# Kernel tuning notes

Measured on AMD Instinct MI355X. Metric: run time of the kernel, lower is better.

## Reference

```python
import jax, jax.numpy as jnp
import numpy as np

B, S, H, T, N = 32, 512, 1024, 8, 16


def setup_inputs() -> dict:
    key = jax.random.key(0)
    ks = jax.random.split(key, 16)
    sc = 1.0 / np.sqrt(H)
    f32 = jnp.float32
    return {
        "hidden": jax.random.normal(ks[0], (S, B, H), f32),
        "num_encoder_outputs": jax.random.normal(ks[1], (B, N, H), f32),
        "problem_q": jax.random.normal(ks[2], (B, H), f32),
        # GenerateXQs K/V projections
        "Wk": jax.random.normal(ks[3], (H, H), f32) * sc,
        "bk": jax.random.normal(ks[4], (H,), f32) * sc,
        "Wv": jax.random.normal(ks[5], (H, H), f32) * sc,
        "bv": jax.random.normal(ks[6], (H,), f32) * sc,
        # XToQ K/V projections
        "Wk2": jax.random.normal(ks[7], (H, H), f32) * sc,
        "bk2": jax.random.normal(ks[8], (H,), f32) * sc,
        "Wv2": jax.random.normal(ks[9], (H, H), f32) * sc,
        "bv2": jax.random.normal(ks[10], (H,), f32) * sc,
        # XToQ single-layer LSTM (PyTorch gate order i,f,g,o)
        "W_ih": jax.random.normal(ks[11], (4 * H, H), f32) * sc,
        "W_hh": jax.random.normal(ks[12], (4 * H, H), f32) * sc,
        "b_ih": jax.random.normal(ks[13], (4 * H,), f32) * sc,
        "b_hh": jax.random.normal(ks[14], (4 * H,), f32) * sc,
        "num_xs": T,  # all batch items generate T tokens (required for torch.stack)
    }


def _attend(x_bh, keys_bsh, values_bsh):
    # softmax(x @ K^T) @ V, batched over b
    scores = jnp.einsum("bh,bsh->bs", x_bh, keys_bsh)
    attn = jax.nn.softmax(scores, axis=-1)
    return jnp.einsum("bs,bsh->bh", attn, values_bsh)


def reference(hidden, num_encoder_outputs, problem_q,
              Wk, bk, Wv, bv, Wk2, bk2, Wv2, bv2,
              W_ih, W_hh, b_ih, b_hh, num_xs):
    Tn = int(num_xs)
    hidden2 = jnp.swapaxes(hidden, 0, 1)           # [B,S,H]
    keys = hidden2 @ Wk.T + bk                      # [B,S,H]
    values = hidden2 @ Wv.T + bv                    # [B,S,H]

    def gen_step(x, _):
        xn = _attend(x, keys, values)
        return xn, xn

    if Tn > 1:
        _, rest = jax.lax.scan(gen_step, problem_q, None, length=Tn - 1)  # [T-1,B,H]
        final_xs = jnp.concatenate(
            [problem_q[:, None, :], jnp.swapaxes(rest, 0, 1)], axis=1)    # [B,T,H]
    else:
        final_xs = problem_q[:, None, :]

    # XToQ: parallel attention of each generated x over the (projected) hidden
    keys2 = hidden2 @ Wk2.T + bk2
    values2 = hidden2 @ Wv2.T + bv2
    scores = jnp.einsum("bth,bsh->bts", final_xs, keys2)
    attn = jax.nn.softmax(scores, axis=-1)
    qs = jnp.einsum("bts,bsh->bth", attn, values2)  # [B,T,H]

    if Tn > 1:
        # single-layer LSTM over time (PyTorch gate order: i, f, g, o)
        def lstm_step(carry, x_t):
            h, c = carry
            gates = x_t @ W_ih.T + b_ih + h @ W_hh.T + b_hh  # [B,4H]
            i, f, g, o = jnp.split(gates, 4, axis=-1)
            i, f, o = jax.nn.sigmoid(i), jax.nn.sigmoid(f), jax.nn.sigmoid(o)
            g = jnp.tanh(g)
            c = f * c + i * g
            h = o * jnp.tanh(c)
            return (h, c), h

        h0 = jnp.zeros((qs.shape[0], H), qs.dtype)
        c0 = jnp.zeros((qs.shape[0], H), qs.dtype)
        _, outs = jax.lax.scan(lstm_step, (h0, c0), jnp.swapaxes(qs, 0, 1))  # [T,B,H]
        # original appends out1[0] (the t=0 LSTM output) as an extra token
        final_qs = jnp.concatenate([qs, outs[0][:, None, :]], axis=1)        # [B,T+1,H]
    else:
        final_qs = qs

    updated_hidden = jnp.swapaxes(jnp.concatenate([hidden2, final_xs], axis=1), 0, 1)  # [S+T,B,H]
    updated_nums = jnp.concatenate([num_encoder_outputs, final_xs], axis=1)             # [B,N+T,H]
    return (final_qs, updated_hidden, updated_nums)
```

## Files before the change

kernel.cpp:

```cpp
#include <hip/hip_runtime.h>
#include <math.h>

#define Bn 32
#define Sn 512
#define Hn 1024
#define Tn 8
#define Nn 16
#define Gn 4096

__device__ __forceinline__ float wsum(float v){
#pragma unroll
  for (int off = 32; off; off >>= 1) v += __shfl_xor(v, off);
  return v;
}

__device__ __forceinline__ float dot16(float4 a0, float4 a1, float4 a2, float4 a3,
                                       float4 v0, float4 v1, float4 v2, float4 v3){
  float d = a0.x*v0.x + a0.y*v0.y + a0.z*v0.z + a0.w*v0.w;
  d += a1.x*v1.x + a1.y*v1.y + a1.z*v1.z + a1.w*v1.w;
  d += a2.x*v2.x + a2.y*v2.y + a2.z*v2.z + a2.w*v2.w;
  d += a3.x*v3.x + a3.y*v3.y + a3.z*v3.z + a3.w*v3.w;
  return d;
}


__global__ __launch_bounds__(256) void transpose3(
    const float* __restrict__ Wk, const float* __restrict__ Wk2, const float* __restrict__ Wv,
    float* __restrict__ WkT, float* __restrict__ Wk2T, float* __restrict__ WvT){
  __shared__ float tile[32][33];
  const float* in  = (blockIdx.z == 0) ? Wk  : (blockIdx.z == 1) ? Wk2  : Wv;
  float*       outp= (blockIdx.z == 0) ? WkT : (blockIdx.z == 1) ? Wk2T : WvT;
  int tx = threadIdx.x & 31, ty = threadIdx.x >> 5;
  int c0 = blockIdx.x * 32, r0 = blockIdx.y * 32;
#pragma unroll
  for (int k = 0; k < 4; ++k)
    tile[ty + 8*k][tx] = in[(size_t)(r0 + ty + 8*k) * Hn + c0 + tx];
  __syncthreads();
#pragma unroll
  for (int k = 0; k < 4; ++k)
    outp[(size_t)(c0 + ty + 8*k) * Hn + r0 + tx] = tile[tx][ty + 8*k];
}

__global__ __launch_bounds__(256) void prep(
    const float4* __restrict__ nums, const float4* __restrict__ pq,
    float4* __restrict__ un, float4* __restrict__ xs){
  int n = blockIdx.x, b = blockIdx.y;
  if (n < Nn) un[((size_t)b*(Nn+Tn) + n)*256 + threadIdx.x] = nums[((size_t)b*Nn + n)*256 + threadIdx.x];
  else        xs[((size_t)b*Tn)*256 + threadIdx.x] = pq[(size_t)b*256 + threadIdx.x];
}

__global__ __launch_bounds__(256) void finalize_xs(const float4* __restrict__ xs, float4* __restrict__ uh, float4* __restrict__ un){
  int t = blockIdx.x, b = blockIdx.y;
  float4 v = xs[((size_t)b*Tn + t)*256 + threadIdx.x];
  uh[(((size_t)(Sn + t))*Bn + b)*256 + threadIdx.x] = v;
  un[((size_t)b*(Nn+Tn) + Nn + t)*256 + threadIdx.x] = v;
}

__global__ __launch_bounds__(256) void dkv(
    const float* __restrict__ bv, const float* __restrict__ WkT, float* __restrict__ dk)
{
  int lane = threadIdx.x & 63, w = threadIdx.x >> 6;
  int j = blockIdx.x*4 + w;
  const float4* rp = (const float4*)(WkT + (size_t)j*Hn) + lane;
  const float4* bp = (const float4*)bv + lane;
  float4 v0=rp[0], v1=rp[64], v2=rp[128], v3=rp[192];
  float4 b0=bp[0], b1=bp[64], b2=bp[128], b3=bp[192];
  float d = wsum(dot16(b0,b1,b2,b3, v0,v1,v2,v3));
  if (lane == 0) dk[j] = d;
}

template<int FIRST>
__global__ __launch_bounds__(512, 4) void attend10(
    const float* __restrict__ hidden, const float* __restrict__ partq,
    const float* __restrict__ dk,
    float* __restrict__ ctxp, float* __restrict__ mlp, float* __restrict__ uh)
{
  const int b = blockIdx.y, p = blockIdx.x;
  const int tid = threadIdx.x, lane = tid & 63, w = tid >> 6;
  __shared__ float xq[1024];
  __shared__ float sM[8], sL[8];
  __shared__ float sacc[8*1024];

  const int s0 = p*32 + w*4;
  size_t ro[4];
#pragma unroll
  for (int i = 0; i < 4; ++i) ro[i] = ((size_t)(s0+i)*Bn + b)*Hn;
  float4 u[4][4];
#pragma unroll
  for (int i = 0; i < 4; ++i){
    const float4* rp = (const float4*)(hidden + ro[i]) + lane;
    u[i][0]=rp[0]; u[i][1]=rp[64]; u[i][2]=rp[128]; u[i][3]=rp[192];
  }

#pragma unroll
  for (int h0 = 0; h0 < 1024; h0 += 512){
    int c = h0 + tid;
    float s = dk ? dk[c] : 0.f;
#pragma unroll
    for (int i = 0; i < 16; ++i) s += partq[((size_t)(i*Bn + b))*1024 + c];
    xq[c] = s;
  }
  if (FIRST){
#pragma unroll
    for (int i = 0; i < 4; ++i){
      float4* wp = (float4*)(uh + ro[i]) + lane;
      wp[0]=u[i][0]; wp[64]=u[i][1]; wp[128]=u[i][2]; wp[192]=u[i][3];
    }
  }
  __syncthreads();
  const float4* xp = (const float4*)xq + lane;
  float4 q0 = xp[0], q1 = xp[64], q2 = xp[128], q3 = xp[192];

  float d[4];
#pragma unroll
  for (int i = 0; i < 4; ++i) d[i] = dot16(q0,q1,q2,q3, u[i][0],u[i][1],u[i][2],u[i][3]);
#pragma unroll
  for (int off = 32; off; off >>= 1){
#pragma unroll
    for (int i = 0; i < 4; ++i) d[i] += __shfl_xor(d[i], off);
  }
  float mw = fmaxf(fmaxf(d[0], d[1]), fmaxf(d[2], d[3]));
  sM[w] = mw;
  __syncthreads();
  float M = sM[0];
#pragma unroll
  for (int i = 1; i < 8; ++i) M = fmaxf(M, sM[i]);
  float wi[4], lw = 0.f;
#pragma unroll
  for (int i = 0; i < 4; ++i){ wi[i] = __expf(d[i] - M); lw += wi[i]; }
  float4 a0, a1, a2, a3;
  a0 = make_float4(wi[0]*u[0][0].x, wi[0]*u[0][0].y, wi[0]*u[0][0].z, wi[0]*u[0][0].w);
  a1 = make_float4(wi[0]*u[0][1].x, wi[0]*u[0][1].y, wi[0]*u[0][1].z, wi[0]*u[0][1].w);
  a2 = make_float4(wi[0]*u[0][2].x, wi[0]*u[0][2].y, wi[0]*u[0][2].z, wi[0]*u[0][2].w);
  a3 = make_float4(wi[0]*u[0][3].x, wi[0]*u[0][3].y, wi[0]*u[0][3].z, wi[0]*u[0][3].w);
#pragma unroll
  for (int i = 1; i < 4; ++i){
    a0.x = fmaf(wi[i], u[i][0].x, a0.x); a0.y = fmaf(wi[i], u[i][0].y, a0.y);
    a0.z = fmaf(wi[i], u[i][0].z, a0.z); a0.w = fmaf(wi[i], u[i][0].w, a0.w);
    a1.x = fmaf(wi[i], u[i][1].x, a1.x); a1.y = fmaf(wi[i], u[i][1].y, a1.y);
    a1.z = fmaf(wi[i], u[i][1].z, a1.z); a1.w = fmaf(wi[i], u[i][1].w, a1.w);
    a2.x = fmaf(wi[i], u[i][2].x, a2.x); a2.y = fmaf(wi[i], u[i][2].y, a2.y);
    a2.z = fmaf(wi[i], u[i][2].z, a2.z); a2.w = fmaf(wi[i], u[i][2].w, a2.w);
    a3.x = fmaf(wi[i], u[i][3].x, a3.x); a3.y = fmaf(wi[i], u[i][3].y, a3.y);
    a3.z = fmaf(wi[i], u[i][3].z, a3.z); a3.w = fmaf(wi[i], u[i][3].w, a3.w);
  }
  {
    int sl0 = (lane*4 + 0) ^ (lane & 7);
    int sl1 = (lane*4 + 1) ^ (lane & 7);
    int sl2 = (lane*4 + 2) ^ (lane & 7);
    int sl3 = (lane*4 + 3) ^ (lane & 7);
    *(float4*)(sacc + w*1024 + sl0*4) = a0;
    *(float4*)(sacc + w*1024 + sl1*4) = a1;
    *(float4*)(sacc + w*1024 + sl2*4) = a2;
    *(float4*)(sacc + w*1024 + sl3*4) = a3;
  }
  if (lane == 0) sL[w] = lw;
  __syncthreads();
#pragma unroll
  for (int h0 = 0; h0 < 1024; h0 += 512){
    int c = h0 + tid;
    int k = c >> 8, l = (c >> 2) & 63, j = c & 3;
    int fo = ((((l << 2) + k) ^ (l & 7)) << 2) + j;
    float s = 0.f;
#pragma unroll
    for (int i = 0; i < 8; ++i) s += sacc[i*1024 + fo];
    ctxp[((size_t)b*16 + p)*1024 + c] = s;
  }
  if (tid == 0){
    float L = 0.f;
#pragma unroll
    for (int i = 0; i < 8; ++i) L += sL[i];
    mlp[((size_t)b*16 + p)*2]     = M;
    mlp[((size_t)b*16 + p)*2 + 1] = L;
  }
}

__global__ __launch_bounds__(256) void mv1(
    const float* __restrict__ X, int xstride,
    const float* __restrict__ M, float* __restrict__ part,
    int nj, int ktiles)
{
  __shared__ float wt[64*128];
  __shared__ float xl[64*32];
  const int t  = threadIdx.x;
  const int j0 = blockIdx.x * 128;
  const int kb = blockIdx.y;
  const int r0 = blockIdx.z * 32;
  const int R  = gridDim.z * 32;
  const int tj = t & 31, tr = t >> 5;
  float acc[4][4] = {{0.f,0.f,0.f,0.f},{0.f,0.f,0.f,0.f},{0.f,0.f,0.f,0.f},{0.f,0.f,0.f,0.f}};

  for (int kt = 0; kt < ktiles; ++kt){
    const int k0 = (kb*ktiles + kt)*64;
    __syncthreads();
    {
      int j = t >> 1;
      int kqb = (t & 1) * 8;
      const float* Mrow = M + (size_t)(j0 + j)*1024 + k0;
#pragma unroll
      for (int c = 0; c < 8; ++c){
        float4 v = *(const float4*)(Mrow + (kqb + c)*4);
        int kk = (kqb + c)*4;
        wt[(kk+0)*128 + j] = v.x;
        wt[(kk+1)*128 + j] = v.y;
        wt[(kk+2)*128 + j] = v.z;
        wt[(kk+3)*128 + j] = v.w;
      }
      int r = t >> 3;
      int kq0 = t & 7;
#pragma unroll
      for (int c = 0; c < 2; ++c){
        int kk = (kq0 + c*8)*4;
        float4 v = *(const float4*)(X + (size_t)(r0 + r)*xstride + k0 + kk);
        xl[(kk+0)*32 + r] = v.x;
        xl[(kk+1)*32 + r] = v.y;
        xl[(kk+2)*32 + r] = v.z;
        xl[(kk+3)*32 + r] = v.w;
      }
    }
    __syncthreads();
#pragma unroll 4
    for (int k = 0; k < 64; ++k){
      float4 w4 = *(const float4*)(wt + k*128 + tj*4);
      float4 x4 = *(const float4*)(xl + k*32  + tr*4);
      acc[0][0] = fmaf(x4.x, w4.x, acc[0][0]);
      acc[0][1] = fmaf(x4.x, w4.y, acc[0][1]);
      acc[0][2] = fmaf(x4.x, w4.z, acc[0][2]);
      acc[0][3] = fmaf(x4.x, w4.w, acc[0][3]);
      acc[1][0] = fmaf(x4.y, w4.x, acc[1][0]);
      acc[1][1] = fmaf(x4.y, w4.y, acc[1][1]);
      acc[1][2] = fmaf(x4.y, w4.z, acc[1][2]);
      acc[1][3] = fmaf(x4.y, w4.w, acc[1][3]);
      acc[2][0] = fmaf(x4.z, w4.x, acc[2][0]);
      acc[2][1] = fmaf(x4.z, w4.y, acc[2][1]);
      acc[2][2] = fmaf(x4.z, w4.z, acc[2][2]);
      acc[2][3] = fmaf(x4.z, w4.w, acc[2][3]);
      acc[3][0] = fmaf(x4.w, w4.x, acc[3][0]);
      acc[3][1] = fmaf(x4.w, w4.y, acc[3][1]);
      acc[3][2] = fmaf(x4.w, w4.z, acc[3][2]);
      acc[3][3] = fmaf(x4.w, w4.w, acc[3][3]);
    }
  }
  const size_t base = ((size_t)kb*R + r0 + tr*4)*nj + j0 + tj*4;
#pragma unroll
  for (int i = 0; i < 4; ++i)
    *(float4*)(part + base + (size_t)i*nj) = make_float4(acc[i][0], acc[i][1], acc[i][2], acc[i][3]);
}

__global__ __launch_bounds__(256) void mv2(
    const float* __restrict__ part, int R, int njshift, int KB,
    const float* __restrict__ b1, const float* __restrict__ b2,
    float* __restrict__ out, int rpgshift, int opg)
{
  int idx = blockIdx.x*256 + threadIdx.x;
  int nj = 1 << njshift;
  int r = idx >> njshift, j = idx & (nj - 1);
  float s = 0.f;
  if (b1) s += b1[j];
  if (b2) s += b2[j];
  size_t stride = (size_t)R << njshift;
  for (int kb = 0; kb < KB; ++kb) s += part[(size_t)kb*stride + idx];
  int orow = ((r >> rpgshift) * opg) + (r & ((1 << rpgshift) - 1));
  out[((size_t)orow << njshift) + j] = s;
}

template<int FULL>
__global__ __launch_bounds__(256) void genw(
    const float* __restrict__ ctxp, const float* __restrict__ mlp,
    const float* __restrict__ D, float* __restrict__ part, float* __restrict__ ctxout)
{
  __shared__ float wt[64*128];
  __shared__ float xl[64*32];
  const int t  = threadIdx.x;
  const int j0 = blockIdx.x * 128;
  const int kb = blockIdx.y;
  const int k0 = kb*64;
  const int tj = t & 31, tr = t >> 5;

  if (FULL){
    int j = t >> 1;
    int kqb = (t & 1) * 8;
    const float* Mrow = D + (size_t)(j0 + j)*1024 + k0;
#pragma unroll
    for (int c = 0; c < 8; ++c){
      float4 v = *(const float4*)(Mrow + (kqb + c)*4);
      int kk = (kqb + c)*4;
      wt[(kk+0)*128 + j] = v.x;
      wt[(kk+1)*128 + j] = v.y;
      wt[(kk+2)*128 + j] = v.z;
      wt[(kk+3)*128 + j] = v.w;
    }
  }
  {
    int b = t >> 3, kk = (t & 7)*8;
    float mx = -1e30f;
#pragma unroll
    for (int i = 0; i < 16; ++i) mx = fmaxf(mx, mlp[((size_t)b*16 + i)*2]);
    float L = 0.f;
    float a8[8] = {0.f,0.f,0.f,0.f,0.f,0.f,0.f,0.f};
#pragma unroll 4
    for (int i = 0; i < 16; ++i){
      float m = mlp[((size_t)b*16 + i)*2];
      float l = mlp[((size_t)b*16 + i)*2 + 1];
      float we = __expf(m - mx);
      L = fmaf(l, we, L);
      const float* cp = ctxp + ((size_t)b*16 + i)*1024 + k0 + kk;
      float4 u0 = *(const float4*)cp;
      float4 u1 = *(const float4*)(cp + 4);
      a8[0] = fmaf(we, u0.x, a8[0]); a8[1] = fmaf(we, u0.y, a8[1]);
      a8[2] = fmaf(we, u0.z, a8[2]); a8[3] = fmaf(we, u0.w, a8[3]);
      a8[4] = fmaf(we, u1.x, a8[4]); a8[5] = fmaf(we, u1.y, a8[5]);
      a8[6] = fmaf(we, u1.z, a8[6]); a8[7] = fmaf(we, u1.w, a8[7]);
    }
    float inv = 1.f / L;
#pragma unroll
    for (int q = 0; q < 8; ++q){
      float c = a8[q]*inv;
      if (FULL) xl[(kk + q)*32 + b] = c;
      if (!FULL || blockIdx.x == 0) ctxout[(size_t)b*1024 + k0 + kk + q] = c;
    }
  }
  if (!FULL) return;
  __syncthreads();
  float acc[4][4] = {{0.f,0.f,0.f,0.f},{0.f,0.f,0.f,0.f},{0.f,0.f,0.f,0.f},{0.f,0.f,0.f,0.f}};
#pragma unroll 4
  for (int k = 0; k < 64; ++k){
    float4 w4 = *(const float4*)(wt + k*128 + tj*4);
    float4 x4 = *(const float4*)(xl + k*32  + tr*4);
    acc[0][0] = fmaf(x4.x, w4.x, acc[0][0]);
    acc[0][1] = fmaf(x4.x, w4.y, acc[0][1]);
    acc[0][2] = fmaf(x4.x, w4.z, acc[0][2]);
    acc[0][3] = fmaf(x4.x, w4.w, acc[0][3]);
    acc[1][0] = fmaf(x4.y, w4.x, acc[1][0]);
    acc[1][1] = fmaf(x4.y, w4.y, acc[1][1]);
    acc[1][2] = fmaf(x4.y, w4.z, acc[1][2]);
    acc[1][3] = fmaf(x4.y, w4.w, acc[1][3]);
    acc[2][0] = fmaf(x4.z, w4.x, acc[2][0]);
    acc[2][1] = fmaf(x4.z, w4.y, acc[2][1]);
    acc[2][2] = fmaf(x4.z, w4.z, acc[2][2]);
    acc[2][3] = fmaf(x4.z, w4.w, acc[2][3]);
    acc[3][0] = fmaf(x4.w, w4.x, acc[3][0]);
    acc[3][1] = fmaf(x4.w, w4.y, acc[3][1]);
    acc[3][2] = fmaf(x4.w, w4.z, acc[3][2]);
    acc[3][3] = fmaf(x4.w, w4.w, acc[3][3]);
  }
  const size_t base = ((size_t)kb*32 + tr*4)*1024 + j0 + tj*4;
#pragma unroll
  for (int i = 0; i < 4; ++i)
    *(float4*)(part + base + (size_t)i*1024) = make_float4(acc[i][0], acc[i][1], acc[i][2], acc[i][3]);
}

__global__ __launch_bounds__(256) void mv2xs(
    const float* __restrict__ part, const float* __restrict__ bv, float* __restrict__ xs)
{
  int idx = blockIdx.x*256 + threadIdx.x;
  int r = idx >> 10, j = idx & 1023;
  int t = r >> 5, b = r & 31;
  const size_t stride = (size_t)224*1024;
  float s = bv[j];
#pragma unroll
  for (int kb = 0; kb < 16; ++kb) s += part[(size_t)kb*stride + idx];
  xs[(((size_t)b*Tn) + t + 1)*1024 + j] = s;
}


__global__ __launch_bounds__(512) void scores2_kernel(
    const float* __restrict__ hidden, const float* __restrict__ xk2, float* __restrict__ sc)
{
  int b = blockIdx.y, p = blockIdx.x;
  int lane = threadIdx.x & 63, w = threadIdx.x >> 6;
  int t0 = (w & 3) * 2, rh = w >> 2;
  const float4* qa = (const float4*)(xk2 + ((size_t)b*Tn + t0  )*Hn) + lane;
  const float4* qb = (const float4*)(xk2 + ((size_t)b*Tn + t0+1)*Hn) + lane;
  float4 a0=qa[0], a1=qa[64], a2=qa[128], a3=qa[192];
  float4 c0=qb[0], c1=qb[64], c2=qb[128], c3=qb[192];
#pragma unroll 2
  for (int r = 0; r < 8; ++r){
    int s = p*16 + rh*8 + r;
    const float4* row = (const float4*)(hidden + ((size_t)s*Bn + b)*Hn) + lane;
    float4 v0=row[0], v1=row[64], v2=row[128], v3=row[192];
    float d0 = wsum(dot16(a0,a1,a2,a3, v0,v1,v2,v3));
    float d1 = wsum(dot16(c0,c1,c2,c3, v0,v1,v2,v3));
    if (lane == 0){
      sc[((size_t)b*Tn + t0  )*Sn + s] = d0;
      sc[((size_t)b*Tn + t0+1)*Sn + s] = d1;
    }
  }
}

__global__ __launch_bounds__(512) void softmax512(float* __restrict__ sc){
  int row = blockIdx.x, tid = threadIdx.x, lane = tid & 63, w = tid >> 6;
  float v = sc[(size_t)row*Sn + tid];
  float mx = v;
#pragma unroll
  for (int off = 32; off; off >>= 1) mx = fmaxf(mx, __shfl_xor(mx, off));
  __shared__ float sm[8], ss[8];
  if (lane == 0) sm[w] = mx;
  __syncthreads();
  mx = sm[0];
#pragma unroll
  for (int i = 1; i < 8; ++i) mx = fmaxf(mx, sm[i]);
  float e = __expf(v - mx);
  float s = e;
#pragma unroll
  for (int off = 32; off; off >>= 1) s += __shfl_xor(s, off);
  if (lane == 0) ss[w] = s;
  __syncthreads();
  float tot = 0.f;
#pragma unroll
  for (int i = 0; i < 8; ++i) tot += ss[i];
  sc[(size_t)row*Sn + tid] = e / tot;
}

__global__ __launch_bounds__(512) void ctx2p(
    const float* __restrict__ hidden, const float* __restrict__ attn, float* __restrict__ part)
{
  int hc = blockIdx.x, sc = blockIdx.y, b = blockIdx.z;
  int tid = threadIdx.x, hloc = tid & 127, tg = tid >> 7;
  __shared__ float al[Tn*128];
  for (int idx = tid; idx < Tn*128; idx += 512){
    int t = idx >> 7, si = idx & 127;
    al[idx] = attn[((size_t)b*Tn + t)*Sn + sc*128 + si];
  }
  __syncthreads();
  int h = hc*128 + hloc, t0 = tg*2;
  float acc0 = 0.f, acc1 = 0.f;
#pragma unroll 4
  for (int si = 0; si < 128; ++si){
    int s = sc*128 + si;
    float v = hidden[((size_t)s*Bn + b)*Hn + h];
    acc0 = fmaf(al[t0*128 + si],     v, acc0);
    acc1 = fmaf(al[(t0+1)*128 + si], v, acc1);
  }
  part[(((size_t)sc*Bn + b)*Tn + t0  )*Hn + h] = acc0;
  part[(((size_t)sc*Bn + b)*Tn + t0+1)*Hn + h] = acc1;
}

__global__ __launch_bounds__(256) void ctx2r(const float* __restrict__ part, float* __restrict__ out){
  int idx = blockIdx.x*256 + threadIdx.x;
  out[idx] = part[idx] + part[262144 + idx] + part[524288 + idx] + part[786432 + idx];
}

__global__ __launch_bounds__(256) void lstm_fused(
    const float* __restrict__ part, const float* __restrict__ b_ih,
    const float* __restrict__ b_hh, float* __restrict__ fq)
{
  int idx = blockIdx.x*256 + threadIdx.x;
  int b = idx >> 10, h = idx & 1023;
  const size_t stride = (size_t)32*Gn;
  float gi = b_ih[h] + b_hh[h];
  float gg = b_ih[2048+h] + b_hh[2048+h];
  float go = b_ih[3072+h] + b_hh[3072+h];
  for (int kb = 0; kb < 16; ++kb){
    const float* pp = part + (size_t)kb*stride + (size_t)b*Gn;
    gi += pp[h]; gg += pp[2048+h]; go += pp[3072+h];
  }
  float si = 1.f/(1.f + __expf(-gi));
  float so = 1.f/(1.f + __expf(-go));
  float c  = si * tanhf(gg);
  fq[((size_t)b*(Tn+1) + Tn)*Hn + h] = so * tanhf(c);
}


extern "C" void kernel_launch(void* const* d_in, const int* in_sizes, int n_in,
                              void* d_out, int out_size, void* d_ws, size_t ws_size,
                              hipStream_t stream) {
  const float* hidden = (const float*)d_in[0];
  const float* nums   = (const float*)d_in[1];
  const float* pq     = (const float*)d_in[2];
  const float* Wk     = (const float*)d_in[3];
  const float* Wv     = (const float*)d_in[5];
  const float* bv     = (const float*)d_in[6];
  const float* Wk2    = (const float*)d_in[7];
  const float* Wv2    = (const float*)d_in[9];
  const float* bv2    = (const float*)d_in[10];
  const float* W_ih   = (const float*)d_in[11];
  const float* b_ih   = (const float*)d_in[13];
  const float* b_hh   = (const float*)d_in[14];

  float* out = (float*)d_out;
  float* fq  = out;
  float* uh  = out + (size_t)Bn*(Tn+1)*Hn;
  float* un  = uh + (size_t)(Sn+Tn)*Bn*Hn;

  float* ws    = (float*)d_ws;
  float* xs    = ws;
  float* ctxp  = ws + 262144;
  float* mlp   = ws + 1310720;
  float* xk2   = ws + 1345536;
  float* sc2   = ws + 1607680;
  float* ctx2v = ws + 1738752;
  float* partX = ws + 2000896;
  float* partK = ws + 2525184;
  float* WkT   = ws + 3049472;
  float* Wk2T  = ws + 4098048;
  float* WvT   = ws + 5146624;
  float* Dcomb = ws + 6195200;
  float* ctxall= ws + 7243776;
  float* dk    = ws + 7473152;
  float* Dparts= ws + 7474176;
  float* c2part= partX;
  float* partL = WkT;

  transpose3<<<dim3(32,32,3), 256, 0, stream>>>(Wk, Wk2, Wv, WkT, Wk2T, WvT);
  prep<<<dim3(Nn+1, Bn), 256, 0, stream>>>((const float4*)nums, (const float4*)pq, (float4*)un, (float4*)xs);
  mv1<<<dim3(8,4,32), 256, 0, stream>>>(WkT, Hn, WvT, Dparts, Hn, 4);
  mv2<<<4096, 256, 0, stream>>>(Dparts, 1024, 10, 4, nullptr, nullptr, Dcomb, 0, 1);
  dkv<<<256, 256, 0, stream>>>(bv, WkT, dk);

  mv1<<<dim3(8,16,1), 256, 0, stream>>>(pq, Hn, WkT, partK, Hn, 1);

  for (int t = 1; t < Tn; ++t){
    if (t == 1) attend10<1><<<dim3(16,Bn), 512, 0, stream>>>(hidden, partK, nullptr, ctxp, mlp, uh);
    else        attend10<0><<<dim3(16,Bn), 512, 0, stream>>>(hidden, partX, dk, ctxp, mlp, uh);
    float* ctxt = ctxall + (size_t)(t-1)*Bn*Hn;
    if (t < Tn-1) genw<1><<<dim3(8,16), 256, 0, stream>>>(ctxp, mlp, Dcomb, partX, ctxt);
    else          genw<0><<<dim3(1,16), 256, 0, stream>>>(ctxp, mlp, Dcomb, partX, ctxt);
  }

  mv1<<<dim3(8,16,7), 256, 0, stream>>>(ctxall, Hn, Wv, Dparts, Hn, 1);
  mv2xs<<<896, 256, 0, stream>>>(Dparts, bv, xs);

  mv1<<<dim3(8,16,8), 256, 0, stream>>>(xs, Hn, Wk2T, Dparts, Hn, 1);
  mv2<<<1024, 256, 0, stream>>>(Dparts, 256, 10, 16, nullptr, nullptr, xk2, 0, 1);
  scores2_kernel<<<dim3(32, Bn), 512, 0, stream>>>(hidden, xk2, sc2);
  softmax512<<<Bn*Tn, 512, 0, stream>>>(sc2);
  ctx2p<<<dim3(8, 4, Bn), 512, 0, stream>>>(hidden, sc2, c2part);
  ctx2r<<<1024, 256, 0, stream>>>(c2part, ctx2v);
  mv1<<<dim3(8,16,8), 256, 0, stream>>>(ctx2v, Hn, Wv2, Dparts, Hn, 1);
  mv2<<<1024, 256, 0, stream>>>(Dparts, 256, 10, 16, bv2, nullptr, fq, 3, Tn+1);

  mv1<<<dim3(32,16,1), 256, 0, stream>>>(fq, (Tn+1)*Hn, W_ih, partL, Gn, 1);
  lstm_fused<<<128, 256, 0, stream>>>(partL, b_ih, b_hh, fq);

  finalize_xs<<<dim3(Tn, Bn), 256, 0, stream>>>((const float4*)xs, (float4*)uh, (float4*)un);
}
```

Measured before the change: 339.0 us.

## Fuse small kernels: transpose+prep, reduce+dk, softmax into ctx, partial-sum into matmul

Merges the weight transpose with the input-copy prep kernel, folds the Dcomb partial reduction together with the dk dot product into one launch, and moves the XToQ softmax into the context kernel. The context partials are now summed inside a new mv1 variant as it loads its X tile. The scores kernel is rewritten to stage all T query rows in shared memory and compute all eight dot products per hidden row. The aim is fewer launches and fewer intermediate global round-trips, at the cost of redundant softmax work in each ctx block and a 16KB shared buffer per block.

Result: no change. 344.6 us (+1.7%).

```diff
diff --git a/kernel.cpp b/kernel.cpp
--- a/kernel.cpp
+++ b/kernel.cpp
@@ -23,10 +23,17 @@
   return d;
 }
 
-
-__global__ __launch_bounds__(256) void transpose3(
+__global__ __launch_bounds__(256) void transprep(
     const float* __restrict__ Wk, const float* __restrict__ Wk2, const float* __restrict__ Wv,
-    float* __restrict__ WkT, float* __restrict__ Wk2T, float* __restrict__ WvT){
+    float* __restrict__ WkT, float* __restrict__ Wk2T, float* __restrict__ WvT,
+    const float4* __restrict__ nums, const float4* __restrict__ pq,
+    float4* __restrict__ un, float4* __restrict__ xs){
+  if (blockIdx.z == 3){
+    int n = blockIdx.x, b = blockIdx.y;
+    if (n < Nn) un[((size_t)b*(Nn+Tn) + n)*256 + threadIdx.x] = nums[((size_t)b*Nn + n)*256 + threadIdx.x];
+    else if (n == Nn) xs[((size_t)b*Tn)*256 + threadIdx.x] = pq[(size_t)b*256 + threadIdx.x];
+    return;
+  }
   __shared__ float tile[32][33];
   const float* in  = (blockIdx.z == 0) ? Wk  : (blockIdx.z == 1) ? Wk2  : Wv;
   float*       outp= (blockIdx.z == 0) ? WkT : (blockIdx.z == 1) ? Wk2T : WvT;
@@ -41,14 +48,6 @@
     outp[(size_t)(c0 + ty + 8*k) * Hn + r0 + tx] = tile[tx][ty + 8*k];
 }
 
-__global__ __launch_bounds__(256) void prep(
-    const float4* __restrict__ nums, const float4* __restrict__ pq,
-    float4* __restrict__ un, float4* __restrict__ xs){
-  int n = blockIdx.x, b = blockIdx.y;
-  if (n < Nn) un[((size_t)b*(Nn+Tn) + n)*256 + threadIdx.x] = nums[((size_t)b*Nn + n)*256 + threadIdx.x];
-  else        xs[((size_t)b*Tn)*256 + threadIdx.x] = pq[(size_t)b*256 + threadIdx.x];
-}
-
 __global__ __launch_bounds__(256) void finalize_xs(const float4* __restrict__ xs, float4* __restrict__ uh, float4* __restrict__ un){
   int t = blockIdx.x, b = blockIdx.y;
   float4 v = xs[((size_t)b*Tn + t)*256 + threadIdx.x];
@@ -56,17 +55,25 @@
   un[((size_t)b*(Nn+Tn) + Nn + t)*256 + threadIdx.x] = v;
 }
 
-__global__ __launch_bounds__(256) void dkv(
+__global__ __launch_bounds__(256) void dred(
+    const float* __restrict__ Dparts, float* __restrict__ Dcomb,
     const float* __restrict__ bv, const float* __restrict__ WkT, float* __restrict__ dk)
 {
-  int lane = threadIdx.x & 63, w = threadIdx.x >> 6;
-  int j = blockIdx.x*4 + w;
-  const float4* rp = (const float4*)(WkT + (size_t)j*Hn) + lane;
-  const float4* bp = (const float4*)bv + lane;
-  float4 v0=rp[0], v1=rp[64], v2=rp[128], v3=rp[192];
-  float4 b0=bp[0], b1=bp[64], b2=bp[128], b3=bp[192];
-  float d = wsum(dot16(b0,b1,b2,b3, v0,v1,v2,v3));
-  if (lane == 0) dk[j] = d;
+  if (blockIdx.x < 4096){
+    int idx = blockIdx.x*256 + threadIdx.x;
+    const size_t stride = (size_t)1024*1024;
+    float s = Dparts[idx] + Dparts[stride + idx] + Dparts[2*stride + idx] + Dparts[3*stride + idx];
+    Dcomb[idx] = s;
+  } else {
+    int lane = threadIdx.x & 63, w = threadIdx.x >> 6;
+    int j = (blockIdx.x - 4096)*4 + w;
+    const float4* rp = (const float4*)(WkT + (size_t)j*Hn) + lane;
+    const float4* bp = (const float4*)bv + lane;
+    float4 v0=rp[0], v1=rp[64], v2=rp[128], v3=rp[192];
+    float4 b0=bp[0], b1=bp[64], b2=bp[128], b3=bp[192];
+    float d = wsum(dot16(b0,b1,b2,b3, v0,v1,v2,v3));
+    if (lane == 0) dk[j] = d;
+  }
 }
 
 template<int FIRST>
@@ -247,6 +254,78 @@
     *(float4*)(part + base + (size_t)i*nj) = make_float4(acc[i][0], acc[i][1], acc[i][2], acc[i][3]);
 }
 
+__global__ __launch_bounds__(256) void mv1r4(
+    const float* __restrict__ X,
+    const float* __restrict__ M, float* __restrict__ part)
+{
+  __shared__ float wt[64*128];
+  __shared__ float xl[64*32];
+  const int t  = threadIdx.x;
+  const int j0 = blockIdx.x * 128;
+  const int kb = blockIdx.y;
+  const int r0 = blockIdx.z * 32;
+  const int tj = t & 31, tr = t >> 5;
+  const int k0 = kb*64;
+  float acc[4][4] = {{0.f,0.f,0.f,0.f},{0.f,0.f,0.f,0.f},{0.f,0.f,0.f,0.f},{0.f,0.f,0.f,0.f}};
+  {
+    int j = t >> 1;
+    int kqb = (t & 1) * 8;
+    const float* Mrow = M + (size_t)(j0 + j)*1024 + k0;
+#pragma unroll
+    for (int c = 0; c < 8; ++c){
+      float4 v = *(const float4*)(Mrow + (kqb + c)*4);
+      int kk = (kqb + c)*4;
+      wt[(kk+0)*128 + j] = v.x;
+      wt[(kk+1)*128 + j] = v.y;
+      wt[(kk+2)*128 + j] = v.z;
+      wt[(kk+3)*128 + j] = v.w;
+    }
+    int r = t >> 3;
+    int kq0 = t & 7;
+#pragma unroll
+    for (int c = 0; c < 2; ++c){
+      int kk = (kq0 + c*8)*4;
+      const float* xp = X + (size_t)(r0 + r)*1024 + k0 + kk;
+      float4 v0 = *(const float4*)(xp);
+      float4 v1 = *(const float4*)(xp + 262144);
+      float4 v2 = *(const float4*)(xp + 524288);
+      float4 v3 = *(const float4*)(xp + 786432);
+      float4 v = make_float4(v0.x+v1.x+v2.x+v3.x, v0.y+v1.y+v2.y+v3.y,
+                             v0.z+v1.z+v2.z+v3.z, v0.w+v1.w+v2.w+v3.w);
+      xl[(kk+0)*32 + r] = v.x;
+      xl[(kk+1)*32 + r] = v.y;
+      xl[(kk+2)*32 + r] = v.z;
+      xl[(kk+3)*32 + r] = v.w;
+    }
+  }
+  __syncthreads();
+#pragma unroll 4
+  for (int k = 0; k < 64; ++k){
+    float4 w4 = *(const float4*)(wt + k*128 + tj*4);
+    float4 x4 = *(const float4*)(xl + k*32  + tr*4);
+    acc[0][0] = fmaf(x4.x, w4.x, acc[0][0]);
+    acc[0][1] = fmaf(x4.x, w4.y, acc[0][1]);
+    acc[0][2] = fmaf(x4.x, w4.z, acc[0][2]);
+    acc[0][3] = fmaf(x4.x, w4.w, acc[0][3]);
+    acc[1][0] = fmaf(x4.y, w4.x, acc[1][0]);
+    acc[1][1] = fmaf(x4.y, w4.y, acc[1][1]);
+    acc[1][2] = fmaf(x4.y, w4.z, acc[1][2]);
+    acc[1][3] = fmaf(x4.y, w4.w, acc[1][3]);
+    acc[2][0] = fmaf(x4.z, w4.x, acc[2][0]);
+    acc[2][1] = fmaf(x4.z, w4.y, acc[2][1]);
+    acc[2][2] = fmaf(x4.z, w4.z, acc[2][2]);
+    acc[2][3] = fmaf(x4.z, w4.w, acc[2][3]);
+    acc[3][0] = fmaf(x4.w, w4.x, acc[3][0]);
+    acc[3][1] = fmaf(x4.w, w4.y, acc[3][1]);
+    acc[3][2] = fmaf(x4.w, w4.z, acc[3][2]);
+    acc[3][3] = fmaf(x4.w, w4.w, acc[3][3]);
+  }
+  const size_t base = ((size_t)kb*256 + r0 + tr*4)*1024 + j0 + tj*4;
+#pragma unroll
+  for (int i = 0; i < 4; ++i)
+    *(float4*)(part + base + (size_t)i*1024) = make_float4(acc[i][0], acc[i][1], acc[i][2], acc[i][3]);
+}
+
 __global__ __launch_bounds__(256) void mv2(
     const float* __restrict__ part, int R, int njshift, int KB,
     const float* __restrict__ b1, const float* __restrict__ b2,
@@ -363,82 +442,81 @@
   xs[(((size_t)b*Tn) + t + 1)*1024 + j] = s;
 }
 
-
-__global__ __launch_bounds__(512) void scores2_kernel(
+__global__ __launch_bounds__(512) void scores2f(
     const float* __restrict__ hidden, const float* __restrict__ xk2, float* __restrict__ sc)
 {
-  int b = blockIdx.y, p = blockIdx.x;
-  int lane = threadIdx.x & 63, w = threadIdx.x >> 6;
-  int t0 = (w & 3) * 2, rh = w >> 2;
-  const float4* qa = (const float4*)(xk2 + ((size_t)b*Tn + t0  )*Hn) + lane;
-  const float4* qb = (const float4*)(xk2 + ((size_t)b*Tn + t0+1)*Hn) + lane;
-  float4 a0=qa[0], a1=qa[64], a2=qa[128], a3=qa[192];
-  float4 c0=qb[0], c1=qb[64], c2=qb[128], c3=qb[192];
-#pragma unroll 2
-  for (int r = 0; r < 8; ++r){
-    int s = p*16 + rh*8 + r;
-    const float4* row = (const float4*)(hidden + ((size_t)s*Bn + b)*Hn) + lane;
-    float4 v0=row[0], v1=row[64], v2=row[128], v3=row[192];
-    float d0 = wsum(dot16(a0,a1,a2,a3, v0,v1,v2,v3));
-    float d1 = wsum(dot16(c0,c1,c2,c3, v0,v1,v2,v3));
-    if (lane == 0){
-      sc[((size_t)b*Tn + t0  )*Sn + s] = d0;
-      sc[((size_t)b*Tn + t0+1)*Sn + s] = d1;
-    }
-  }
-}
-
-__global__ __launch_bounds__(512) void softmax512(float* __restrict__ sc){
-  int row = blockIdx.x, tid = threadIdx.x, lane = tid & 63, w = tid >> 6;
-  float v = sc[(size_t)row*Sn + tid];
-  float mx = v;
-#pragma unroll
-  for (int off = 32; off; off >>= 1) mx = fmaxf(mx, __shfl_xor(mx, off));
-  __shared__ float sm[8], ss[8];
-  if (lane == 0) sm[w] = mx;
-  __syncthreads();
-  mx = sm[0];
-#pragma unroll
-  for (int i = 1; i < 8; ++i) mx = fmaxf(mx, sm[i]);
-  float e = __expf(v - mx);
-  float s = e;
-#pragma unroll
-  for (int off = 32; off; off >>= 1) s += __shfl_xor(s, off);
-  if (lane == 0) ss[w] = s;
-  __syncthreads();
-  float tot = 0.f;
-#pragma unroll
-  for (int i = 0; i < 8; ++i) tot += ss[i];
-  sc[(size_t)row*Sn + tid] = e / tot;
-}
-
-__global__ __launch_bounds__(512) void ctx2p(
-    const float* __restrict__ hidden, const float* __restrict__ attn, float* __restrict__ part)
+  const int b = blockIdx.y, p = blockIdx.x;
+  const int tid = threadIdx.x, lane = tid & 63, w = tid >> 6;
+  __shared__ float xq2[Tn*1024];
+
+  const int s0 = p*16 + w*2;
+  size_t r0 = ((size_t)(s0+0)*Bn + b)*Hn, r1 = ((size_t)(s0+1)*Bn + b)*Hn;
+  const float4* rp0 = (const float4*)(hidden + r0) + lane;
+  const float4* rp1 = (const float4*)(hidden + r1) + lane;
+  float4 u0=rp0[0], u1=rp0[64], u2=rp0[128], u3=rp0[192];
+  float4 v0=rp1[0], v1=rp1[64], v2=rp1[128], v3=rp1[192];
+
+  for (int c = tid; c < Tn*1024; c += 512) xq2[c] = xk2[(size_t)b*Tn*1024 + c];
+  __syncthreads();
+
+  float d0[Tn], d1[Tn];
+#pragma unroll
+  for (int q = 0; q < Tn; ++q){
+    const float4* qp = (const float4*)(xq2 + q*1024) + lane;
+    float4 a0=qp[0], a1=qp[64], a2=qp[128], a3=qp[192];
+    d0[q] = dot16(a0,a1,a2,a3, u0,u1,u2,u3);
+    d1[q] = dot16(a0,a1,a2,a3, v0,v1,v2,v3);
+  }
+#pragma unroll
+  for (int off = 32; off; off >>= 1){
+#pragma unroll
+    for (int q = 0; q < Tn; ++q){ d0[q] += __shfl_xor(d0[q], off); d1[q] += __shfl_xor(d1[q], off); }
+  }
+  if (lane == 0){
+#pragma unroll
+    for (int q = 0; q < Tn; ++q){
+      sc[((size_t)b*Tn + q)*Sn + s0    ] = d0[q];
+      sc[((size_t)b*Tn + q)*Sn + s0 + 1] = d1[q];
+    }
+  }
+}
+
+__global__ __launch_bounds__(512) void ctx2pf(
+    const float* __restrict__ hidden, const float* __restrict__ scraw, float* __restrict__ part)
 {
   int hc = blockIdx.x, sc = blockIdx.y, b = blockIdx.z;
-  int tid = threadIdx.x, hloc = tid & 127, tg = tid >> 7;
-  __shared__ float al[Tn*128];
-  for (int idx = tid; idx < Tn*128; idx += 512){
-    int t = idx >> 7, si = idx & 127;
-    al[idx] = attn[((size_t)b*Tn + t)*Sn + sc*128 + si];
-  }
-  __syncthreads();
+  int tid = threadIdx.x, lane = tid & 63, w = tid >> 6;
+  __shared__ float al[Tn*Sn];
+  for (int idx = tid; idx < Tn*Sn; idx += 512) al[idx] = scraw[(size_t)b*Tn*Sn + idx];
+  __syncthreads();
+  {
+    float mx = -1e30f;
+#pragma unroll
+    for (int k = 0; k < 8; ++k) mx = fmaxf(mx, al[w*Sn + lane + k*64]);
+#pragma unroll
+    for (int off = 32; off; off >>= 1) mx = fmaxf(mx, __shfl_xor(mx, off));
+    float e[8], s = 0.f;
+#pragma unroll
+    for (int k = 0; k < 8; ++k){ e[k] = __expf(al[w*Sn + lane + k*64] - mx); s += e[k]; }
+#pragma unroll
+    for (int off = 32; off; off >>= 1) s += __shfl_xor(s, off);
+    float inv = 1.f / s;
+#pragma unroll
+    for (int k = 0; k < 8; ++k) al[w*Sn + lane + k*64] = e[k] * inv;
+  }
+  __syncthreads();
+  int hloc = tid & 127, tg = tid >> 7;
   int h = hc*128 + hloc, t0 = tg*2;
   float acc0 = 0.f, acc1 = 0.f;
 #pragma unroll 4
   for (int si = 0; si < 128; ++si){
     int s = sc*128 + si;
     float v = hidden[((size_t)s*Bn + b)*Hn + h];
-    acc0 = fmaf(al[t0*128 + si],     v, acc0);
-    acc1 = fmaf(al[(t0+1)*128 + si], v, acc1);
+    acc0 = fmaf(al[t0*Sn + s],     v, acc0);
+    acc1 = fmaf(al[(t0+1)*Sn + s], v, acc1);
   }
   part[(((size_t)sc*Bn + b)*Tn + t0  )*Hn + h] = acc0;
   part[(((size_t)sc*Bn + b)*Tn + t0+1)*Hn + h] = acc1;
-}
-
-__global__ __launch_bounds__(256) void ctx2r(const float* __restrict__ part, float* __restrict__ out){
-  int idx = blockIdx.x*256 + threadIdx.x;
-  out[idx] = part[idx] + part[262144 + idx] + part[524288 + idx] + part[786432 + idx];
 }
 
 __global__ __launch_bounds__(256) void lstm_fused(
@@ -489,7 +567,6 @@
   float* mlp   = ws + 1310720;
   float* xk2   = ws + 1345536;
   float* sc2   = ws + 1607680;
-  float* ctx2v = ws + 1738752;
   float* partX = ws + 2000896;
   float* partK = ws + 2525184;
   float* WkT   = ws + 3049472;
@@ -502,11 +579,10 @@
   float* c2part= partX;
   float* partL = WkT;
 
-  transpose3<<<dim3(32,32,3), 256, 0, stream>>>(Wk, Wk2, Wv, WkT, Wk2T, WvT);
-  prep<<<dim3(Nn+1, Bn), 256, 0, stream>>>((const float4*)nums, (const float4*)pq, (float4*)un, (float4*)xs);
+  transprep<<<dim3(32,32,4), 256, 0, stream>>>(Wk, Wk2, Wv, WkT, Wk2T, WvT,
+      (const float4*)nums, (const float4*)pq, (float4*)un, (float4*)xs);
   mv1<<<dim3(8,4,32), 256, 0, stream>>>(WkT, Hn, WvT, Dparts, Hn, 4);
-  mv2<<<4096, 256, 0, stream>>>(Dparts, 1024, 10, 4, nullptr, nullptr, Dcomb, 0, 1);
-  dkv<<<256, 256, 0, stream>>>(bv, WkT, dk);
+  dred<<<4352, 256, 0, stream>>>(Dparts, Dcomb, bv, WkT, dk);
 
   mv1<<<dim3(8,16,1), 256, 0, stream>>>(pq, Hn, WkT, partK, Hn, 1);
 
@@ -523,11 +599,9 @@
 
   mv1<<<dim3(8,16,8), 256, 0, stream>>>(xs, Hn, Wk2T, Dparts, Hn, 1);
   mv2<<<1024, 256, 0, stream>>>(Dparts, 256, 10, 16, nullptr, nullptr, xk2, 0, 1);
-  scores2_kernel<<<dim3(32, Bn), 512, 0, stream>>>(hidden, xk2, sc2);
-  softmax512<<<Bn*Tn, 512, 0, stream>>>(sc2);
-  ctx2p<<<dim3(8, 4, Bn), 512, 0, stream>>>(hidden, sc2, c2part);
-  ctx2r<<<1024, 256, 0, stream>>>(c2part, ctx2v);
-  mv1<<<dim3(8,16,8), 256, 0, stream>>>(ctx2v, Hn, Wv2, Dparts, Hn, 1);
+  scores2f<<<dim3(32, Bn), 512, 0, stream>>>(hidden, xk2, sc2);
+  ctx2pf<<<dim3(8, 4, Bn), 512, 0, stream>>>(hidden, sc2, c2part);
+  mv1r4<<<dim3(8,16,8), 256, 0, stream>>>(c2part, Wv2, Dparts);
   mv2<<<1024, 256, 0, stream>>>(Dparts, 256, 10, 16, bv2, nullptr, fq, 3, Tn+1);
 
   mv1<<<dim3(32,16,1), 256, 0, stream>>>(fq, (Tn+1)*Hn, W_ih, partL, Gn, 1);
```

## Fuse softmax combine and D projection into attention via per-batch spin barrier

Applied to the files above, without the earlier changes.

The attention kernel is restructured so that the 16 blocks of each batch item sync through an atomic counter and spin-wait. After the sync, each block merges the partial softmax stats and contexts, writes the context, and computes its 64-wide slice of the next query with a per-row D matvec. This removes the separate genw launch and the partial-sum reduction at each step. Setup kernels are also merged (transpose with prep, D reduction with dk) to cut launch count. In exchange, the code relies on all 16 blocks of a batch being co-resident, has a bounded spin as fallback, and each batch re-reads the full D matrix instead of sharing it across batches in a tiled GEMM.

Result: slower. 438.5 us (+29.3%).

```diff
diff --git a/kernel.cpp b/kernel.cpp
--- a/kernel.cpp
+++ b/kernel.cpp
@@ -23,10 +23,17 @@
   return d;
 }
 
-
-__global__ __launch_bounds__(256) void transpose3(
+__global__ __launch_bounds__(256) void transprep(
     const float* __restrict__ Wk, const float* __restrict__ Wk2, const float* __restrict__ Wv,
-    float* __restrict__ WkT, float* __restrict__ Wk2T, float* __restrict__ WvT){
+    float* __restrict__ WkT, float* __restrict__ Wk2T, float* __restrict__ WvT,
+    const float4* __restrict__ nums, const float4* __restrict__ pq,
+    float4* __restrict__ un, float4* __restrict__ xs){
+  if (blockIdx.z == 3){
+    int n = blockIdx.x, b = blockIdx.y;
+    if (n < Nn) un[((size_t)b*(Nn+Tn) + n)*256 + threadIdx.x] = nums[((size_t)b*Nn + n)*256 + threadIdx.x];
+    else if (n == Nn) xs[((size_t)b*Tn)*256 + threadIdx.x] = pq[(size_t)b*256 + threadIdx.x];
+    return;
+  }
   __shared__ float tile[32][33];
   const float* in  = (blockIdx.z == 0) ? Wk  : (blockIdx.z == 1) ? Wk2  : Wv;
   float*       outp= (blockIdx.z == 0) ? WkT : (blockIdx.z == 1) ? Wk2T : WvT;
@@ -41,14 +48,6 @@
     outp[(size_t)(c0 + ty + 8*k) * Hn + r0 + tx] = tile[tx][ty + 8*k];
 }
 
-__global__ __launch_bounds__(256) void prep(
-    const float4* __restrict__ nums, const float4* __restrict__ pq,
-    float4* __restrict__ un, float4* __restrict__ xs){
-  int n = blockIdx.x, b = blockIdx.y;
-  if (n < Nn) un[((size_t)b*(Nn+Tn) + n)*256 + threadIdx.x] = nums[((size_t)b*Nn + n)*256 + threadIdx.x];
-  else        xs[((size_t)b*Tn)*256 + threadIdx.x] = pq[(size_t)b*256 + threadIdx.x];
-}
-
 __global__ __launch_bounds__(256) void finalize_xs(const float4* __restrict__ xs, float4* __restrict__ uh, float4* __restrict__ un){
   int t = blockIdx.x, b = blockIdx.y;
   float4 v = xs[((size_t)b*Tn + t)*256 + threadIdx.x];
@@ -56,30 +55,48 @@
   un[((size_t)b*(Nn+Tn) + Nn + t)*256 + threadIdx.x] = v;
 }
 
-__global__ __launch_bounds__(256) void dkv(
+__global__ __launch_bounds__(256) void dred(
+    const float* __restrict__ Dparts, float* __restrict__ Dcomb,
     const float* __restrict__ bv, const float* __restrict__ WkT, float* __restrict__ dk)
 {
-  int lane = threadIdx.x & 63, w = threadIdx.x >> 6;
-  int j = blockIdx.x*4 + w;
-  const float4* rp = (const float4*)(WkT + (size_t)j*Hn) + lane;
-  const float4* bp = (const float4*)bv + lane;
-  float4 v0=rp[0], v1=rp[64], v2=rp[128], v3=rp[192];
-  float4 b0=bp[0], b1=bp[64], b2=bp[128], b3=bp[192];
-  float d = wsum(dot16(b0,b1,b2,b3, v0,v1,v2,v3));
-  if (lane == 0) dk[j] = d;
-}
-
-template<int FIRST>
-__global__ __launch_bounds__(512, 4) void attend10(
-    const float* __restrict__ hidden, const float* __restrict__ partq,
-    const float* __restrict__ dk,
-    float* __restrict__ ctxp, float* __restrict__ mlp, float* __restrict__ uh)
-{
-  const int b = blockIdx.y, p = blockIdx.x;
+  if (blockIdx.x < 4096){
+    int idx = blockIdx.x*256 + threadIdx.x;
+    const size_t stride = (size_t)1024*1024;
+    float s = Dparts[idx] + Dparts[stride + idx] + Dparts[2*stride + idx] + Dparts[3*stride + idx];
+    Dcomb[idx] = s;
+  } else {
+    int lane = threadIdx.x & 63, w = threadIdx.x >> 6;
+    int j = (blockIdx.x - 4096)*4 + w;
+    const float4* rp = (const float4*)(WkT + (size_t)j*Hn) + lane;
+    const float4* bp = (const float4*)bv + lane;
+    float4 v0=rp[0], v1=rp[64], v2=rp[128], v3=rp[192];
+    float4 b0=bp[0], b1=bp[64], b2=bp[128], b3=bp[192];
+    float d = wsum(dot16(b0,b1,b2,b3, v0,v1,v2,v3));
+    if (lane == 0) dk[j] = d;
+  }
+}
+
+__global__ void zcnt(unsigned* __restrict__ cnt){
+  cnt[(size_t)threadIdx.x * 16] = 0u;
+}
+
+template<int FIRST, int LAST>
+__global__ __launch_bounds__(512, 4) void attend11(
+    const float* __restrict__ hidden, const float* __restrict__ xkq_in,
+    const float* __restrict__ dk, const float* __restrict__ D,
+    float* __restrict__ ctxp, float* __restrict__ mlp,
+    float* __restrict__ xkq_out, float* __restrict__ ctxout,
+    unsigned* __restrict__ cnt, float* __restrict__ uh)
+{
+  const int bid = blockIdx.x;
+  const int p = bid & 15, b = bid >> 4;
   const int tid = threadIdx.x, lane = tid & 63, w = tid >> 6;
-  __shared__ float xq[1024];
+  __shared__ float sacc[8*1024];
+  __shared__ float ctxs[1024];
   __shared__ float sM[8], sL[8];
-  __shared__ float sacc[8*1024];
+
+  const float4* xp = (const float4*)(xkq_in + (size_t)b*Hn) + lane;
+  float4 q0 = xp[0], q1 = xp[64], q2 = xp[128], q3 = xp[192];
 
   const int s0 = p*32 + w*4;
   size_t ro[4];
@@ -90,15 +107,6 @@
   for (int i = 0; i < 4; ++i){
     const float4* rp = (const float4*)(hidden + ro[i]) + lane;
     u[i][0]=rp[0]; u[i][1]=rp[64]; u[i][2]=rp[128]; u[i][3]=rp[192];
-  }
-
-#pragma unroll
-  for (int h0 = 0; h0 < 1024; h0 += 512){
-    int c = h0 + tid;
-    float s = dk ? dk[c] : 0.f;
-#pragma unroll
-    for (int i = 0; i < 16; ++i) s += partq[((size_t)(i*Bn + b))*1024 + c];
-    xq[c] = s;
   }
   if (FIRST){
 #pragma unroll
@@ -107,10 +115,6 @@
       wp[0]=u[i][0]; wp[64]=u[i][1]; wp[128]=u[i][2]; wp[192]=u[i][3];
     }
   }
-  __syncthreads();
-  const float4* xp = (const float4*)xq + lane;
-  float4 q0 = xp[0], q1 = xp[64], q2 = xp[128], q3 = xp[192];
-
   float d[4];
 #pragma unroll
   for (int i = 0; i < 4; ++i) d[i] = dot16(q0,q1,q2,q3, u[i][0],u[i][1],u[i][2],u[i][3]);
@@ -171,7 +175,53 @@
 #pragma unroll
     for (int i = 0; i < 8; ++i) L += sL[i];
     mlp[((size_t)b*16 + p)*2]     = M;
-    mlp[((size_t)b*16 + p)*2 + 1] = L;
+    mlp[((size_t)b*16 + p)*2 + 1] = lw*0.f + L;
+  }
+
+  __syncthreads();
+  if (tid == 0){
+    __threadfence();
+    atomicAdd(cnt + (size_t)b*16, 1u);
+    unsigned it = 0;
+    while (atomicAdd(cnt + (size_t)b*16, 0u) < 16u && it < (1u<<20)){
+      ++it;
+      __builtin_amdgcn_s_sleep(2);
+    }
+  }
+  __syncthreads();
+
+  float wex[16];
+  float M2 = -1e30f, Lc = 0.f;
+#pragma unroll
+  for (int i = 0; i < 16; ++i) M2 = fmaxf(M2, mlp[((size_t)b*16 + i)*2]);
+#pragma unroll
+  for (int i = 0; i < 16; ++i){
+    float e = __expf(mlp[((size_t)b*16 + i)*2] - M2);
+    wex[i] = e;
+    Lc = fmaf(mlp[((size_t)b*16 + i)*2 + 1], e, Lc);
+  }
+  float inv = 1.f / Lc;
+#pragma unroll
+  for (int h0 = 0; h0 < 1024; h0 += 512){
+    int c = h0 + tid;
+    float s = 0.f;
+#pragma unroll
+    for (int i = 0; i < 16; ++i) s = fmaf(wex[i], ctxp[((size_t)b*16 + i)*1024 + c], s);
+    ctxs[c] = s * inv;
+  }
+  __syncthreads();
+  if (tid < 64) ctxout[(size_t)b*Hn + p*64 + tid] = ctxs[p*64 + tid];
+  if (!LAST){
+    const float4* cx = (const float4*)ctxs + lane;
+    float4 c0 = cx[0], c1 = cx[64], c2 = cx[128], c3 = cx[192];
+#pragma unroll
+    for (int jj = 0; jj < 8; ++jj){
+      int j = p*64 + w*8 + jj;
+      const float4* Dr = (const float4*)(D + (size_t)j*Hn) + lane;
+      float4 e0 = Dr[0], e1 = Dr[64], e2 = Dr[128], e3 = Dr[192];
+      float s = wsum(dot16(c0,c1,c2,c3, e0,e1,e2,e3));
+      if (lane == 0) xkq_out[(size_t)b*Hn + j] = s + dk[j];
+    }
   }
 }
 
@@ -264,92 +314,6 @@
   out[((size_t)orow << njshift) + j] = s;
 }
 
-template<int FULL>
-__global__ __launch_bounds__(256) void genw(
-    const float* __restrict__ ctxp, const float* __restrict__ mlp,
-    const float* __restrict__ D, float* __restrict__ part, float* __restrict__ ctxout)
-{
-  __shared__ float wt[64*128];
-  __shared__ float xl[64*32];
-  const int t  = threadIdx.x;
-  const int j0 = blockIdx.x * 128;
-  const int kb = blockIdx.y;
-  const int k0 = kb*64;
-  const int tj = t & 31, tr = t >> 5;
-
-  if (FULL){
-    int j = t >> 1;
-    int kqb = (t & 1) * 8;
-    const float* Mrow = D + (size_t)(j0 + j)*1024 + k0;
-#pragma unroll
-    for (int c = 0; c < 8; ++c){
-      float4 v = *(const float4*)(Mrow + (kqb + c)*4);
-      int kk = (kqb + c)*4;
-      wt[(kk+0)*128 + j] = v.x;
-      wt[(kk+1)*128 + j] = v.y;
-      wt[(kk+2)*128 + j] = v.z;
-      wt[(kk+3)*128 + j] = v.w;
-    }
-  }
-  {
-    int b = t >> 3, kk = (t & 7)*8;
-    float mx = -1e30f;
-#pragma unroll
-    for (int i = 0; i < 16; ++i) mx = fmaxf(mx, mlp[((size_t)b*16 + i)*2]);
-    float L = 0.f;
-    float a8[8] = {0.f,0.f,0.f,0.f,0.f,0.f,0.f,0.f};
-#pragma unroll 4
-    for (int i = 0; i < 16; ++i){
-      float m = mlp[((size_t)b*16 + i)*2];
-      float l = mlp[((size_t)b*16 + i)*2 + 1];
-      float we = __expf(m - mx);
-      L = fmaf(l, we, L);
-      const float* cp = ctxp + ((size_t)b*16 + i)*1024 + k0 + kk;
-      float4 u0 = *(const float4*)cp;
-      float4 u1 = *(const float4*)(cp + 4);
-      a8[0] = fmaf(we, u0.x, a8[0]); a8[1] = fmaf(we, u0.y, a8[1]);
-      a8[2] = fmaf(we, u0.z, a8[2]); a8[3] = fmaf(we, u0.w, a8[3]);
-      a8[4] = fmaf(we, u1.x, a8[4]); a8[5] = fmaf(we, u1.y, a8[5]);
-      a8[6] = fmaf(we, u1.z, a8[6]); a8[7] = fmaf(we, u1.w, a8[7]);
-    }
-    float inv = 1.f / L;
-#pragma unroll
-    for (int q = 0; q < 8; ++q){
-      float c = a8[q]*inv;
-      if (FULL) xl[(kk + q)*32 + b] = c;
-      if (!FULL || blockIdx.x == 0) ctxout[(size_t)b*1024 + k0 + kk + q] = c;
-    }
-  }
-  if (!FULL) return;
-  __syncthreads();
-  float acc[4][4] = {{0.f,0.f,0.f,0.f},{0.f,0.f,0.f,0.f},{0.f,0.f,0.f,0.f},{0.f,0.f,0.f,0.f}};
-#pragma unroll 4
-  for (int k = 0; k < 64; ++k){
-    float4 w4 = *(const float4*)(wt + k*128 + tj*4);
-    float4 x4 = *(const float4*)(xl + k*32  + tr*4);
-    acc[0][0] = fmaf(x4.x, w4.x, acc[0][0]);
-    acc[0][1] = fmaf(x4.x, w4.y, acc[0][1]);
-    acc[0][2] = fmaf(x4.x, w4.z, acc[0][2]);
-    acc[0][3] = fmaf(x4.x, w4.w, acc[0][3]);
-    acc[1][0] = fmaf(x4.y, w4.x, acc[1][0]);
-    acc[1][1] = fmaf(x4.y, w4.y, acc[1][1]);
-    acc[1][2] = fmaf(x4.y, w4.z, acc[1][2]);
-    acc[1][3] = fmaf(x4.y, w4.w, acc[1][3]);
-    acc[2][0] = fmaf(x4.z, w4.x, acc[2][0]);
-    acc[2][1] = fmaf(x4.z, w4.y, acc[2][1]);
-    acc[2][2] = fmaf(x4.z, w4.z, acc[2][2]);
-    acc[2][3] = fmaf(x4.z, w4.w, acc[2][3]);
-    acc[3][0] = fmaf(x4.w, w4.x, acc[3][0]);
-    acc[3][1] = fmaf(x4.w, w4.y, acc[3][1]);
-    acc[3][2] = fmaf(x4.w, w4.z, acc[3][2]);
-    acc[3][3] = fmaf(x4.w, w4.w, acc[3][3]);
-  }
-  const size_t base = ((size_t)kb*32 + tr*4)*1024 + j0 + tj*4;
-#pragma unroll
-  for (int i = 0; i < 4; ++i)
-    *(float4*)(part + base + (size_t)i*1024) = make_float4(acc[i][0], acc[i][1], acc[i][2], acc[i][3]);
-}
-
 __global__ __launch_bounds__(256) void mv2xs(
     const float* __restrict__ part, const float* __restrict__ bv, float* __restrict__ xs)
 {
@@ -499,23 +463,28 @@
   float* ctxall= ws + 7243776;
   float* dk    = ws + 7473152;
   float* Dparts= ws + 7474176;
+  float* xkq   = ws + 11668480;
+  unsigned* cnt= (unsigned*)(ws + 11701248);
   float* c2part= partX;
   float* partL = WkT;
 
-  transpose3<<<dim3(32,32,3), 256, 0, stream>>>(Wk, Wk2, Wv, WkT, Wk2T, WvT);
-  prep<<<dim3(Nn+1, Bn), 256, 0, stream>>>((const float4*)nums, (const float4*)pq, (float4*)un, (float4*)xs);
+  transprep<<<dim3(32,32,4), 256, 0, stream>>>(Wk, Wk2, Wv, WkT, Wk2T, WvT,
+      (const float4*)nums, (const float4*)pq, (float4*)un, (float4*)xs);
   mv1<<<dim3(8,4,32), 256, 0, stream>>>(WkT, Hn, WvT, Dparts, Hn, 4);
-  mv2<<<4096, 256, 0, stream>>>(Dparts, 1024, 10, 4, nullptr, nullptr, Dcomb, 0, 1);
-  dkv<<<256, 256, 0, stream>>>(bv, WkT, dk);
-
+  dred<<<4352, 256, 0, stream>>>(Dparts, Dcomb, bv, WkT, dk);
   mv1<<<dim3(8,16,1), 256, 0, stream>>>(pq, Hn, WkT, partK, Hn, 1);
+  mv2<<<128, 256, 0, stream>>>(partK, 32, 10, 16, nullptr, nullptr, xkq, 0, 1);
+  zcnt<<<1, 224, 0, stream>>>(cnt);
 
   for (int t = 1; t < Tn; ++t){
-    if (t == 1) attend10<1><<<dim3(16,Bn), 512, 0, stream>>>(hidden, partK, nullptr, ctxp, mlp, uh);
-    else        attend10<0><<<dim3(16,Bn), 512, 0, stream>>>(hidden, partX, dk, ctxp, mlp, uh);
     float* ctxt = ctxall + (size_t)(t-1)*Bn*Hn;
-    if (t < Tn-1) genw<1><<<dim3(8,16), 256, 0, stream>>>(ctxp, mlp, Dcomb, partX, ctxt);
-    else          genw<0><<<dim3(1,16), 256, 0, stream>>>(ctxp, mlp, Dcomb, partX, ctxt);
+    unsigned* cs = cnt + (size_t)(t-1)*32*16;
+    if (t == 1)
+      attend11<1,0><<<512, 512, 0, stream>>>(hidden, xkq, dk, Dcomb, ctxp, mlp, xkq, ctxt, cs, uh);
+    else if (t < Tn-1)
+      attend11<0,0><<<512, 512, 0, stream>>>(hidden, xkq, dk, Dcomb, ctxp, mlp, xkq, ctxt, cs, uh);
+    else
+      attend11<0,1><<<512, 512, 0, stream>>>(hidden, xkq, dk, Dcomb, ctxp, mlp, xkq, ctxt, cs, uh);
   }
 
   mv1<<<dim3(8,16,7), 256, 0, stream>>>(ctxall, Hn, Wv, Dparts, Hn, 1);
```
